# Kernel optimization log

Hardware: AMD Instinct MI355X
Metric: run time of the kernel (lower is better)

Reference implementation:

```python
import jax, jax.numpy as jnp
import numpy as np

GAMMA = 0.1
PENALTY = 0.0
BANDWIDTH = 1.0e6
B, N, M = 64, 512, 512


def setup_inputs() -> dict:
    key = jax.random.key(0)
    k1, k2, k3 = jax.random.split(key, 3)
    D = jax.random.uniform(k1, (B, N, M), dtype=jnp.float32)
    mask = jnp.ones((B, N, M), dtype=jnp.float32)
    # valid lengths in [N/2, N] so R[b, x_lens[b], y_lens[b]] is always reachable
    x_lens = jax.random.randint(k2, (B,), N // 2, N + 1)
    y_lens = jax.random.randint(k3, (B,), M // 2, M + 1)
    return {"D": D, "mask": mask, "x_lens": x_lens, "y_lens": y_lens}


def _softdtw(D, x_lens, y_lens):
    # Soft-DTW DP over anti-diagonals. D: [B, N, M] masked cost.
    # Returns per-batch loss R[b, x_lens[b], y_lens[b]].
    Bn, Nn, Mn = D.shape
    inv_gamma = 1.0 / GAMMA
    inf = jnp.float32(jnp.inf)
    ii = jnp.arange(Nn + 1)  # row index i = 0..N within a diagonal buffer
    im1 = jnp.clip(ii - 1, 0, Nn)
    # diagonal buffers: entry i of diag s holds R[i, s - i]
    d0 = jnp.full((Bn, Nn + 1), inf).at[:, 0].set(0.0)  # s=0: only R[0,0]=0
    d1 = jnp.full((Bn, Nn + 1), inf)                    # s=1: boundary, all inf
    xl = x_lens[:, None]
    yl = y_lens[:, None]

    def step(carry, s):
        dm2, dm1 = carry                      # diagonals s-2 and s-1
        jj = s - ii                           # column index j for each i
        r00 = dm2[:, im1]                     # R[i-1, j-1]
        r01 = dm1[:, im1]                     # R[i-1, j]
        r10 = dm1                             # R[i,   j-1]
        r0 = -r00 * inv_gamma
        r1 = -(r01 + PENALTY) * inv_gamma
        r2 = -(r10 + PENALTY) * inv_gamma
        rmax = jnp.maximum(jnp.maximum(r0, r1), r2)
        finite = jnp.isfinite(rmax)
        rs = jnp.where(finite, rmax, 0.0)     # safe max (avoid inf-inf -> nan)
        rsum = jnp.exp(r0 - rs) + jnp.exp(r1 - rs) + jnp.exp(r2 - rs)
        softmin = jnp.where(finite, -GAMMA * (jnp.log(rsum) + rs), inf)
        dcell = D[:, jnp.clip(ii - 1, 0, Nn - 1), jnp.clip(jj - 1, 0, Mn - 1)]
        new = dcell + softmin                 # R[i, j] = D[i-1, j-1] + softmin
        valid = (ii >= 1) & (ii <= Nn) & (jj >= 1) & (jj <= Mn)
        valid = valid & (jnp.abs(jj - ii) <= BANDWIDTH)
        upd = valid[None, :] & (ii[None, :] <= xl) & (jj[None, :] <= yl)
        dnew = jnp.where(upd, new, inf)
        return (dm1, dnew), dnew

    _, diags = jax.lax.scan(step, (d0, d1), jnp.arange(2, Nn + Mn + 1))
    # diags: [N+M-1, B, N+1]; diag index s-2 holds cells with i+j == s
    s_idx = jnp.clip(x_lens + y_lens - 2, 0, Nn + Mn - 2)
    loss = diags[s_idx, jnp.arange(Bn), x_lens]
    return loss


def reference(D, mask, x_lens, y_lens):
    return _softdtw(D * mask, x_lens, y_lens)
```

## Files before the change

### kernel.cpp

```cpp
#include <hip/hip_runtime.h>


constexpr int Bn = 64, Nn = 512, Mn = 512;
constexpr int TARGET_E = -30;

__device__ __forceinline__ float exp2_fast(float x) {
    float r; asm("v_exp_f32 %0, %1" : "=v"(r) : "v"(x)); return r;
}
__device__ __forceinline__ float log2_fast(float x) {
    float r; asm("v_log_f32 %0, %1" : "=v"(r) : "v"(x)); return r;
}
__device__ __forceinline__ float ldexp_fast(float x, int e) {
    float r; asm("v_ldexp_f32 %0, %1, %2" : "=v"(r) : "v"(x), "v"(e)); return r;
}
__device__ __forceinline__ int frexp_exp(float x) {
    int r; asm("v_frexp_exp_i32_f32 %0, %1" : "=v"(r) : "v"(x)); return r;
}

#define PLOAD(MM)                                                              \
    {   const int base_ = 4 * ((MM) - t);                                      \
        _Pragma("unroll")                                                      \
        for (int rr = 0; rr < 4; ++rr) {                                       \
            int r_ = min(max(base_ + rr, 0), Nn - 1);                          \
            int o_ = r_ * (Mn / 4) + chunk;                                    \
            pD[rr][0] = D4[o_];  pD[rr][1] = D4[o_ + 1];                       \
            pM[rr][0] = M4[o_];  pM[rr][1] = M4[o_ + 1];                       \
        } }

#define PBUILD(MM)                                                             \
    {   const int s_ = (MM) % 6;                                               \
        _Pragma("unroll")                                                      \
        for (int rr = 0; rr < 4; ++rr) {                                       \
            float4 p_ = pD[rr][0] * pM[rr][0] * negk;                          \
            float4 q_ = pD[rr][1] * pM[rr][1] * negk;                          \
            float4 wa_, wb_;                                                   \
            wa_.x = exp2_fast(p_.x);  wa_.y = exp2_fast(p_.y);                 \
            wa_.z = exp2_fast(p_.z);  wa_.w = exp2_fast(p_.w);                 \
            wb_.x = exp2_fast(q_.x);  wb_.y = exp2_fast(q_.y);                 \
            wb_.z = exp2_fast(q_.z);  wb_.w = exp2_fast(q_.w);                 \
            wlds[s_][2 * rr][t]     = wa_;                                     \
            wlds[s_][2 * rr + 1][t] = wb_;                                     \
        } }

#define CSTEP(MM, WCUR, WNXT)                                                  \
    {                                                                          \
        const int m_ = (MM);                                                   \
        {   const int sn_ = (m_ + 1) % 6;                                      \
            _Pragma("unroll")                                                  \
            for (int rr = 0; rr < 4; ++rr) {                                   \
                WNXT[rr][0] = wlds[sn_][2 * rr][t];                            \
                WNXT[rr][1] = wlds[sn_][2 * rr + 1][t];                        \
            } }                                                                \
        if (m_ <= 63) {                                   \
            if (m_ == t && t != 0) {                                           \
                _Pragma("unroll")                                              \
                for (int c = 0; c < 8; ++c) E[c] = 0.0f;                       \
                Ld = 0.0f;                                                     \
            }                                                                  \
        }                                                                      \
        float ce3_, co_[4];                                                    \
        _Pragma("unroll")                                                      \
        for (int rr = 0; rr < 4; ++rr) {                                       \
            const float Wr_[8] = {                                             \
                WCUR[rr][0].x, WCUR[rr][0].y, WCUR[rr][0].z, WCUR[rr][0].w,    \
                WCUR[rr][1].x, WCUR[rr][1].y, WCUR[rr][1].z, WCUR[rr][1].w };  \
            const float c0s_ = (rr == 0) ? Ld : L[rr - 1];                     \
            float c2_ = L[rr];                                                 \
            float A_[8], Bv_[8];                                               \
            A_[0] = E[0] + c0s_;                                               \
            _Pragma("unroll")                                                  \
            for (int c = 1; c < 8; ++c) A_[c] = E[c] + E[c - 1];               \
            _Pragma("unroll")                                                  \
            for (int c = 0; c < 8; ++c) Bv_[c] = Wr_[c] * A_[c];               \
            _Pragma("unroll")                                                  \
            for (int c = 0; c < 8; ++c) {                                      \
                float nv_ = fmaf(Wr_[c], c2_, Bv_[c]);                         \
                E[c] = nv_;  c2_ = nv_;                                        \
            }                                                                  \
            if (rr == 3) ce3_ = c2_;                                           \
            co_[rr] = __shfl_up(c2_, 1);                                       \
            if (m_ == m_out && rr == r_out) {         \
                float sel_ = E[0];                                             \
                if (c_out == 1) sel_ = E[1];  if (c_out == 2) sel_ = E[2];     \
                if (c_out == 3) sel_ = E[3];  if (c_out == 4) sel_ = E[4];     \
                if (c_out == 5) sel_ = E[5];  if (c_out == 6) sel_ = E[6];     \
                if (c_out == 7) sel_ = E[7];                                   \
                ov = sel_;  ovS = S;                                           \
            }                                                                  \
        }                                                                      \
        int So_ = __shfl_up(S, 1);                                             \
        int eo_ = frexp_exp(ce3_);                                             \
        int ei_ = frexp_exp(co_[3]) + (So_ - S);                               \
        bool own0_  = (ce3_ == 0.0f);                                          \
        bool incok_ = (t != 0) && (co_[3] != 0.0f);                            \
        int  eref_  = (incok_ && ((ei_ > eo_) || own0_)) ? ei_ : eo_;          \
        int  shift_ = (own0_ && !incok_) ? 0 : (TARGET_E - eref_);             \
        if (m_ < t) shift_ = S - So_;                \
        int Snew_ = S - shift_;                                                \
        _Pragma("unroll")                                                      \
        for (int c = 0; c < 8; ++c) E[c] = ldexp_fast(E[c], shift_);           \
        Ld = ldexp_fast(L[3], shift_);                                         \
        {   int d_ = So_ - Snew_;                                              \
            _Pragma("unroll")                                                  \
            for (int rr = 0; rr < 4; ++rr)                                     \
                L[rr] = (t == 0) ? 0.0f : ldexp_fast(co_[rr], d_);             \
        }                                                                      \
        S = Snew_;                                                             \
    }

__global__ __launch_bounds__(192) void softdtw_fwd(
    const float* __restrict__ D, const float* __restrict__ Msk,
    const int* __restrict__ xlens, const int* __restrict__ ylens,
    float* __restrict__ out)
{
    const int tid = threadIdx.x;
    const int w   = tid >> 6;
    const int t   = tid & 63;
    const int b   = blockIdx.x;
    const int xl = xlens[b];
    const int yl = ylens[b];
    const int t_out = (yl - 1) >> 3;
    const int c_out = (yl - 1) & 7;
    const int r_out = (xl - 1) & 3;
    const int m_out = ((xl - 1) >> 2) + t_out;
    const int nsuper = (m_out >> 1) + 1;

    const float negk = -14.4269504088896341f;
    const float klog = 0.06931471805599453f;

    __shared__ float4 wlds[6][8][64];

    const float4* __restrict__ D4 = (const float4*)(D   + (size_t)b * (Nn * Mn));
    const float4* __restrict__ M4 = (const float4*)(Msk + (size_t)b * (Nn * Mn));
    const int chunk = t * 2;

    float E[8];
#pragma unroll
    for (int c = 0; c < 8; ++c) E[c] = 0.0f;
    float L[4] = {0.0f, 0.0f, 0.0f, 0.0f};
    float Ld = (t == 0) ? 1.0f : 0.0f;
    int S = 0;
    float ov = 1.0f;  int ovS = 0;
    float4 Wc[4][2], Wn[4][2];

    float4 pD[4][2], pM[4][2];

    if (w == 1) {
        PLOAD(0); PBUILD(0);
        PLOAD(2); PBUILD(2);
        PLOAD(4);
    } else if (w == 2) {
        PLOAD(1); PBUILD(1);
        PLOAD(3); PBUILD(3);
        PLOAD(5);
    }
    __syncthreads();
    if (w == 0) {
#pragma unroll
        for (int rr = 0; rr < 4; ++rr) {
            Wc[rr][0] = wlds[0][2 * rr][t];
            Wc[rr][1] = wlds[0][2 * rr + 1][t];
        }
    }

    for (int u = 0; u < nsuper; ++u) {
        if (w == 0) {
            CSTEP(2 * u, Wc, Wn);
            if (2 * u + 1 <= m_out) CSTEP(2 * u + 1, Wn, Wc);
        } else if (w == 1) {
            PBUILD(2 * u + 4);
            PLOAD(2 * u + 6);
        } else {
            PBUILD(2 * u + 5);
            PLOAD(2 * u + 7);
        }
        __syncthreads();
    }

    if (w == 0 && t == t_out) {
        int   ev = frexp_exp(ov);
        float mv = ldexp_fast(ov, -ev);
        out[b] = -(log2_fast(mv) + (float)(ev + ovS)) * klog;
    }
}

extern "C" void kernel_launch(void* const* d_in, const int* in_sizes, int n_in,
                              void* d_out, int out_size, void* d_ws, size_t ws_size,
                              hipStream_t stream) {
    const float* D   = (const float*)d_in[0];
    const float* Msk = (const float*)d_in[1];
    const int*   xl  = (const int*)d_in[2];
    const int*   yl  = (const int*)d_in[3];
    float* out = (float*)d_out;
    softdtw_fwd<<<dim3(Bn), dim3(192), 0, stream>>>(D, Msk, xl, yl, out);
}
```

Measured before the change: 145.7 us.

## Replace per-step block barriers with LDS flag-based producer/consumer handoff

Result: slower. 172.0 us (+18.1%).

```diff
diff --git a/kernel.cpp b/kernel.cpp
--- a/kernel.cpp
+++ b/kernel.cpp
@@ -17,22 +17,29 @@
     int r; asm("v_frexp_exp_i32_f32 %0, %1" : "=v"(r) : "v"(x)); return r;
 }
 
-#define PLOAD(MM)                                                              \
+#define LGKM0() asm volatile("s_waitcnt lgkmcnt(0)" ::: "memory")
+#define SCHED_FENCE() __builtin_amdgcn_sched_barrier(0)
+
+#define PLOAD(MM, BD, BM)                                                      \
     {   const int base_ = 4 * ((MM) - t);                                      \
         _Pragma("unroll")                                                      \
         for (int rr = 0; rr < 4; ++rr) {                                       \
             int r_ = min(max(base_ + rr, 0), Nn - 1);                          \
             int o_ = r_ * (Mn / 4) + chunk;                                    \
-            pD[rr][0] = D4[o_];  pD[rr][1] = D4[o_ + 1];                       \
-            pM[rr][0] = M4[o_];  pM[rr][1] = M4[o_ + 1];                       \
+            BD[rr][0] = D4[o_];  BD[rr][1] = D4[o_ + 1];                       \
+            BM[rr][0] = M4[o_];  BM[rr][1] = M4[o_ + 1];                       \
         } }
 
-#define PBUILD(MM)                                                             \
-    {   const int s_ = (MM) % 6;                                               \
-        _Pragma("unroll")                                                      \
-        for (int rr = 0; rr < 4; ++rr) {                                       \
-            float4 p_ = pD[rr][0] * pM[rr][0] * negk;                          \
-            float4 q_ = pD[rr][1] * pM[rr][1] * negk;                          \
+#define PSTEP(MM, BD, BM)                                                      \
+    {                                                                          \
+        const int m_ = (MM);                                                   \
+        while (vcd[0] < m_ - 7) {}                                             \
+        SCHED_FENCE();                                                         \
+        const int s_ = m_ % 6;                                                 \
+        _Pragma("unroll")                                                      \
+        for (int rr = 0; rr < 4; ++rr) {                                       \
+            float4 p_ = BD[rr][0] * BM[rr][0] * negk;                          \
+            float4 q_ = BD[rr][1] * BM[rr][1] * negk;                          \
             float4 wa_, wb_;                                                   \
             wa_.x = exp2_fast(p_.x);  wa_.y = exp2_fast(p_.y);                 \
             wa_.z = exp2_fast(p_.z);  wa_.w = exp2_fast(p_.w);                 \
@@ -40,18 +47,24 @@
             wb_.z = exp2_fast(q_.z);  wb_.w = exp2_fast(q_.w);                 \
             wlds[s_][2 * rr][t]     = wa_;                                     \
             wlds[s_][2 * rr + 1][t] = wb_;                                     \
-        } }
+        }                                                                      \
+        LGKM0();                                                               \
+        if (t == 0) vfs[s_] = m_;                                              \
+        PLOAD(m_ + 4, BD, BM);                                                 \
+    }
 
 #define CSTEP(MM, WCUR, WNXT)                                                  \
     {                                                                          \
         const int m_ = (MM);                                                   \
-        {   const int sn_ = (m_ + 1) % 6;                                      \
-            _Pragma("unroll")                                                  \
-            for (int rr = 0; rr < 4; ++rr) {                                   \
-                WNXT[rr][0] = wlds[sn_][2 * rr][t];                            \
-                WNXT[rr][1] = wlds[sn_][2 * rr + 1][t];                        \
-            } }                                                                \
-        if (m_ <= 63) {                                   \
+        const int sn_ = (m_ + 1) % 6;                                          \
+        while (vfs[sn_] != m_ + 1) {}                                          \
+        SCHED_FENCE();                                                         \
+        _Pragma("unroll")                                                      \
+        for (int rr = 0; rr < 4; ++rr) {                                       \
+            WNXT[rr][0] = wlds[sn_][2 * rr][t];                                \
+            WNXT[rr][1] = wlds[sn_][2 * rr + 1][t];                            \
+        }                                                                      \
+        if (m_ <= 63) {                                                        \
             if (m_ == t && t != 0) {                                           \
                 _Pragma("unroll")                                              \
                 for (int c = 0; c < 8; ++c) E[c] = 0.0f;                       \
@@ -106,6 +119,8 @@
                 L[rr] = (t == 0) ? 0.0f : ldexp_fast(co_[rr], d_);             \
         }                                                                      \
         S = Snew_;                                                             \
+        LGKM0();                                                               \
+        if (t == 0) vcd[0] = m_;                                               \
     }
 
 __global__ __launch_bounds__(192) void softdtw_fwd(
@@ -123,64 +138,64 @@
     const int c_out = (yl - 1) & 7;
     const int r_out = (xl - 1) & 3;
     const int m_out = ((xl - 1) >> 2) + t_out;
-    const int nsuper = (m_out >> 1) + 1;
+    const int mlast = m_out + 1;
 
     const float negk = -14.4269504088896341f;
     const float klog = 0.06931471805599453f;
 
     __shared__ float4 wlds[6][8][64];
+    __shared__ int fslot[6];
+    __shared__ int cdone;
+    volatile int* vfs = fslot;
+    volatile int* vcd = &cdone;
+
+    if (tid < 6) fslot[tid] = -1;
+    if (tid == 6) cdone = -1;
+    __syncthreads();
 
     const float4* __restrict__ D4 = (const float4*)(D   + (size_t)b * (Nn * Mn));
     const float4* __restrict__ M4 = (const float4*)(Msk + (size_t)b * (Nn * Mn));
     const int chunk = t * 2;
 
-    float E[8];
+    if (w == 0) {
+        float E[8];
 #pragma unroll
-    for (int c = 0; c < 8; ++c) E[c] = 0.0f;
-    float L[4] = {0.0f, 0.0f, 0.0f, 0.0f};
-    float Ld = (t == 0) ? 1.0f : 0.0f;
-    int S = 0;
-    float ov = 1.0f;  int ovS = 0;
-    float4 Wc[4][2], Wn[4][2];
-
-    float4 pD[4][2], pM[4][2];
-
-    if (w == 1) {
-        PLOAD(0); PBUILD(0);
-        PLOAD(2); PBUILD(2);
-        PLOAD(4);
-    } else if (w == 2) {
-        PLOAD(1); PBUILD(1);
-        PLOAD(3); PBUILD(3);
-        PLOAD(5);
-    }
-    __syncthreads();
-    if (w == 0) {
+        for (int c = 0; c < 8; ++c) E[c] = 0.0f;
+        float L[4] = {0.0f, 0.0f, 0.0f, 0.0f};
+        float Ld = (t == 0) ? 1.0f : 0.0f;
+        int S = 0;
+        float ov = 1.0f;  int ovS = 0;
+        float4 Wc[4][2], Wn[4][2];
+
+        while (vfs[0] != 0) {}
+        SCHED_FENCE();
 #pragma unroll
         for (int rr = 0; rr < 4; ++rr) {
             Wc[rr][0] = wlds[0][2 * rr][t];
             Wc[rr][1] = wlds[0][2 * rr + 1][t];
         }
-    }
-
-    for (int u = 0; u < nsuper; ++u) {
-        if (w == 0) {
-            CSTEP(2 * u, Wc, Wn);
-            if (2 * u + 1 <= m_out) CSTEP(2 * u + 1, Wn, Wc);
-        } else if (w == 1) {
-            PBUILD(2 * u + 4);
-            PLOAD(2 * u + 6);
-        } else {
-            PBUILD(2 * u + 5);
-            PLOAD(2 * u + 7);
-        }
-        __syncthreads();
-    }
-
-    if (w == 0 && t == t_out) {
-        int   ev = frexp_exp(ov);
-        float mv = ldexp_fast(ov, -ev);
-        out[b] = -(log2_fast(mv) + (float)(ev + ovS)) * klog;
+
+        int m = 0;
+        for (; m + 1 <= m_out; m += 2) {
+            CSTEP(m,     Wc, Wn);
+            CSTEP(m + 1, Wn, Wc);
+        }
+        if (m <= m_out) CSTEP(m, Wc, Wn);
+
+        if (t == t_out) {
+            int   ev = frexp_exp(ov);
+            float mv = ldexp_fast(ov, -ev);
+            out[b] = -(log2_fast(mv) + (float)(ev + ovS)) * klog;
+        }
+    } else {
+        const int p = w - 1;
+        float4 pDa[4][2], pMa[4][2], pDb[4][2], pMb[4][2];
+        PLOAD(p,     pDa, pMa);
+        PLOAD(p + 2, pDb, pMb);
+        for (int mp = p; mp <= mlast; mp += 4) {
+            PSTEP(mp, pDa, pMa);
+            if (mp + 2 <= mlast) PSTEP(mp + 2, pDb, pMb);
+        }
     }
 }
 
```

## Widen per-lane tile to 8x8 and use four producer wavefronts

Applied to the files above, without the earlier changes.

Measured after the change: 223.9 us. 53.8% more time.

```diff
diff --git a/kernel.cpp b/kernel.cpp
--- a/kernel.cpp
+++ b/kernel.cpp
@@ -2,7 +2,7 @@
 
 
 constexpr int Bn = 64, Nn = 512, Mn = 512;
-constexpr int TARGET_E = -30;
+constexpr int TARGET_E = -8;
 
 __device__ __forceinline__ float exp2_fast(float x) {
     float r; asm("v_exp_f32 %0, %1" : "=v"(r) : "v"(x)); return r;
@@ -17,50 +17,51 @@
     int r; asm("v_frexp_exp_i32_f32 %0, %1" : "=v"(r) : "v"(x)); return r;
 }
 
-#define PLOAD(MM)                                                              \
-    {   const int base_ = 4 * ((MM) - t);                                      \
+#define PLOAD4(SLOT, RBASE, BD, BM)                                            \
+    {   const int base_ = 8 * ((SLOT) - t) + (RBASE);                          \
         _Pragma("unroll")                                                      \
         for (int rr = 0; rr < 4; ++rr) {                                       \
             int r_ = min(max(base_ + rr, 0), Nn - 1);                          \
             int o_ = r_ * (Mn / 4) + chunk;                                    \
-            pD[rr][0] = D4[o_];  pD[rr][1] = D4[o_ + 1];                       \
-            pM[rr][0] = M4[o_];  pM[rr][1] = M4[o_ + 1];                       \
+            BD[rr][0] = D4[o_];  BD[rr][1] = D4[o_ + 1];                       \
+            BM[rr][0] = M4[o_];  BM[rr][1] = M4[o_ + 1];                       \
         } }
 
-#define PBUILD(MM)                                                             \
-    {   const int s_ = (MM) % 6;                                               \
+#define PBUILD4(SLOT, RBASE, BD, BM)                                           \
+    {   const int s_ = (SLOT) & 3;                                             \
         _Pragma("unroll")                                                      \
         for (int rr = 0; rr < 4; ++rr) {                                       \
-            float4 p_ = pD[rr][0] * pM[rr][0] * negk;                          \
-            float4 q_ = pD[rr][1] * pM[rr][1] * negk;                          \
+            float4 p_ = BD[rr][0] * BM[rr][0] * negk;                          \
+            float4 q_ = BD[rr][1] * BM[rr][1] * negk;                          \
             float4 wa_, wb_;                                                   \
             wa_.x = exp2_fast(p_.x);  wa_.y = exp2_fast(p_.y);                 \
             wa_.z = exp2_fast(p_.z);  wa_.w = exp2_fast(p_.w);                 \
             wb_.x = exp2_fast(q_.x);  wb_.y = exp2_fast(q_.y);                 \
             wb_.z = exp2_fast(q_.z);  wb_.w = exp2_fast(q_.w);                 \
-            wlds[s_][2 * rr][t]     = wa_;                                     \
-            wlds[s_][2 * rr + 1][t] = wb_;                                     \
+            wlds[s_][2 * ((RBASE) + rr)][t]     = wa_;                         \
+            wlds[s_][2 * ((RBASE) + rr) + 1][t] = wb_;                         \
         } }
 
-#define CSTEP(MM, WCUR, WNXT)                                                  \
+#define CSTEP8(MM, WCUR, WNXT)                                                 \
     {                                                                          \
-        const int m_ = (MM);                                                   \
-        {   const int sn_ = (m_ + 1) % 6;                                      \
-            _Pragma("unroll")                                                  \
-            for (int rr = 0; rr < 4; ++rr) {                                   \
-                WNXT[rr][0] = wlds[sn_][2 * rr][t];                            \
-                WNXT[rr][1] = wlds[sn_][2 * rr + 1][t];                        \
-            } }                                                                \
-        if (m_ <= 63) {                                   \
+        const int m_  = (MM);                                                  \
+        const int sn_ = (m_ + 1) & 3;                                          \
+        _Pragma("unroll")                                                      \
+        for (int rr = 0; rr < 8; ++rr) {                                       \
+            WNXT[rr][0] = wlds[sn_][2 * rr][t];                                \
+            WNXT[rr][1] = wlds[sn_][2 * rr + 1][t];                            \
+        }                                                                      \
+        if (m_ <= 63) {                                                        \
             if (m_ == t && t != 0) {                                           \
                 _Pragma("unroll")                                              \
                 for (int c = 0; c < 8; ++c) E[c] = 0.0f;                       \
                 Ld = 0.0f;                                                     \
             }                                                                  \
         }                                                                      \
-        float ce3_, co_[4];                                                    \
-        _Pragma("unroll")                                                      \
-        for (int rr = 0; rr < 4; ++rr) {                                       \
+        float ce7_ = 0.0f;                                                     \
+        float co_[8];                                                          \
+        _Pragma("unroll")                                                      \
+        for (int rr = 0; rr < 8; ++rr) {                                       \
             const float Wr_[8] = {                                             \
                 WCUR[rr][0].x, WCUR[rr][0].y, WCUR[rr][0].z, WCUR[rr][0].w,    \
                 WCUR[rr][1].x, WCUR[rr][1].y, WCUR[rr][1].z, WCUR[rr][1].w };  \
@@ -77,38 +78,40 @@
                 float nv_ = fmaf(Wr_[c], c2_, Bv_[c]);                         \
                 E[c] = nv_;  c2_ = nv_;                                        \
             }                                                                  \
-            if (rr == 3) ce3_ = c2_;                                           \
+            if (rr == 7) ce7_ = c2_;                                           \
             co_[rr] = __shfl_up(c2_, 1);                                       \
-            if (m_ == m_out && rr == r_out) {         \
-                float sel_ = E[0];                                             \
-                if (c_out == 1) sel_ = E[1];  if (c_out == 2) sel_ = E[2];     \
-                if (c_out == 3) sel_ = E[3];  if (c_out == 4) sel_ = E[4];     \
-                if (c_out == 5) sel_ = E[5];  if (c_out == 6) sel_ = E[6];     \
-                if (c_out == 7) sel_ = E[7];                                   \
-                ov = sel_;  ovS = S;                                           \
+            if (m_ == m_out) {                       \
+                if (rr == r_out) {                                             \
+                    float sel_ = E[0];                                         \
+                    if (c_out == 1) sel_ = E[1];  if (c_out == 2) sel_ = E[2]; \
+                    if (c_out == 3) sel_ = E[3];  if (c_out == 4) sel_ = E[4]; \
+                    if (c_out == 5) sel_ = E[5];  if (c_out == 6) sel_ = E[6]; \
+                    if (c_out == 7) sel_ = E[7];                               \
+                    ov = sel_;  ovS = S;                                       \
+                }                                                              \
             }                                                                  \
         }                                                                      \
         int So_ = __shfl_up(S, 1);                                             \
-        int eo_ = frexp_exp(ce3_);                                             \
-        int ei_ = frexp_exp(co_[3]) + (So_ - S);                               \
-        bool own0_  = (ce3_ == 0.0f);                                          \
-        bool incok_ = (t != 0) && (co_[3] != 0.0f);                            \
+        int eo_ = frexp_exp(ce7_);                                             \
+        int ei_ = frexp_exp(co_[7]) + (So_ - S);                               \
+        bool own0_  = (ce7_ == 0.0f);                                          \
+        bool incok_ = (t != 0) && (co_[7] != 0.0f);                            \
         int  eref_  = (incok_ && ((ei_ > eo_) || own0_)) ? ei_ : eo_;          \
         int  shift_ = (own0_ && !incok_) ? 0 : (TARGET_E - eref_);             \
         if (m_ < t) shift_ = S - So_;                \
         int Snew_ = S - shift_;                                                \
         _Pragma("unroll")                                                      \
         for (int c = 0; c < 8; ++c) E[c] = ldexp_fast(E[c], shift_);           \
-        Ld = ldexp_fast(L[3], shift_);                                         \
+        Ld = ldexp_fast(L[7], shift_);                                         \
         {   int d_ = So_ - Snew_;                                              \
             _Pragma("unroll")                                                  \
-            for (int rr = 0; rr < 4; ++rr)                                     \
+            for (int rr = 0; rr < 8; ++rr)                                     \
                 L[rr] = (t == 0) ? 0.0f : ldexp_fast(co_[rr], d_);             \
         }                                                                      \
         S = Snew_;                                                             \
     }
 
-__global__ __launch_bounds__(192) void softdtw_fwd(
+__global__ __launch_bounds__(320, 1) void softdtw_fwd(
     const float* __restrict__ D, const float* __restrict__ Msk,
     const int* __restrict__ xlens, const int* __restrict__ ylens,
     float* __restrict__ out)
@@ -121,14 +124,14 @@
     const int yl = ylens[b];
     const int t_out = (yl - 1) >> 3;
     const int c_out = (yl - 1) & 7;
-    const int r_out = (xl - 1) & 3;
-    const int m_out = ((xl - 1) >> 2) + t_out;
+    const int r_out = (xl - 1) & 7;
+    const int m_out = ((xl - 1) >> 3) + t_out;
     const int nsuper = (m_out >> 1) + 1;
 
     const float negk = -14.4269504088896341f;
     const float klog = 0.06931471805599453f;
 
-    __shared__ float4 wlds[6][8][64];
+    __shared__ float4 wlds[4][16][64];
 
     const float4* __restrict__ D4 = (const float4*)(D   + (size_t)b * (Nn * Mn));
     const float4* __restrict__ M4 = (const float4*)(Msk + (size_t)b * (Nn * Mn));
@@ -137,27 +140,29 @@
     float E[8];
 #pragma unroll
     for (int c = 0; c < 8; ++c) E[c] = 0.0f;
-    float L[4] = {0.0f, 0.0f, 0.0f, 0.0f};
+    float L[8] = {0.0f, 0.0f, 0.0f, 0.0f, 0.0f, 0.0f, 0.0f, 0.0f};
     float Ld = (t == 0) ? 1.0f : 0.0f;
     int S = 0;
     float ov = 1.0f;  int ovS = 0;
-    float4 Wc[4][2], Wn[4][2];
-
-    float4 pD[4][2], pM[4][2];
-
-    if (w == 1) {
-        PLOAD(0); PBUILD(0);
-        PLOAD(2); PBUILD(2);
-        PLOAD(4);
-    } else if (w == 2) {
-        PLOAD(1); PBUILD(1);
-        PLOAD(3); PBUILD(3);
-        PLOAD(5);
+    float4 Wc[8][2], Wn[8][2];
+
+    const int q    = w - 1;
+    const int half = (q & 1) * 4;
+    const int ss   = q >> 1;
+    float4 bD0[4][2], bM0[4][2], bD1[4][2], bM1[4][2];
+
+    if (w != 0) {
+        if (q < 3) {
+            PLOAD4(q, 0, bD0, bM0);  PBUILD4(q, 0, bD0, bM0);
+            PLOAD4(q, 4, bD0, bM0);  PBUILD4(q, 4, bD0, bM0);
+        }
+        PLOAD4(3 + ss, half, bD1, bM1);
     }
     __syncthreads();
+
     if (w == 0) {
 #pragma unroll
-        for (int rr = 0; rr < 4; ++rr) {
+        for (int rr = 0; rr < 8; ++rr) {
             Wc[rr][0] = wlds[0][2 * rr][t];
             Wc[rr][1] = wlds[0][2 * rr + 1][t];
         }
@@ -165,14 +170,13 @@
 
     for (int u = 0; u < nsuper; ++u) {
         if (w == 0) {
-            CSTEP(2 * u, Wc, Wn);
-            if (2 * u + 1 <= m_out) CSTEP(2 * u + 1, Wn, Wc);
-        } else if (w == 1) {
-            PBUILD(2 * u + 4);
-            PLOAD(2 * u + 6);
+            CSTEP8(2 * u, Wc, Wn);
+            if (2 * u + 1 <= m_out) CSTEP8(2 * u + 1, Wn, Wc);
         } else {
-            PBUILD(2 * u + 5);
-            PLOAD(2 * u + 7);
+            if (u & 1) { PLOAD4(2 * u + 5 + ss, half, bD1, bM1);
+                         PBUILD4(2 * u + 3 + ss, half, bD0, bM0); }
+            else       { PLOAD4(2 * u + 5 + ss, half, bD0, bM0);
+                         PBUILD4(2 * u + 3 + ss, half, bD1, bM1); }
         }
         __syncthreads();
     }
@@ -192,5 +196,5 @@
     const int*   xl  = (const int*)d_in[2];
     const int*   yl  = (const int*)d_in[3];
     float* out = (float*)d_out;
-    softdtw_fwd<<<dim3(Bn), dim3(192), 0, stream>>>(D, Msk, xl, yl, out);
-}
+    softdtw_fwd<<<dim3(Bn), dim3(320), 0, stream>>>(D, Msk, xl, yl, out);
+}
```

## Double-buffer producer global loads and defer consumer LDS prefetch past compute

Applied to the files above, without the earlier changes.

Measured after the change: 155.5 us. +6.8%, slower.

```diff
diff --git a/kernel.cpp b/kernel.cpp
--- a/kernel.cpp
+++ b/kernel.cpp
@@ -17,22 +17,22 @@
     int r; asm("v_frexp_exp_i32_f32 %0, %1" : "=v"(r) : "v"(x)); return r;
 }
 
-#define PLOAD(MM)                                                              \
+#define PLOAD(MM, BD, BM)                                                      \
     {   const int base_ = 4 * ((MM) - t);                                      \
         _Pragma("unroll")                                                      \
         for (int rr = 0; rr < 4; ++rr) {                                       \
             int r_ = min(max(base_ + rr, 0), Nn - 1);                          \
             int o_ = r_ * (Mn / 4) + chunk;                                    \
-            pD[rr][0] = D4[o_];  pD[rr][1] = D4[o_ + 1];                       \
-            pM[rr][0] = M4[o_];  pM[rr][1] = M4[o_ + 1];                       \
+            BD[rr][0] = D4[o_];  BD[rr][1] = D4[o_ + 1];                       \
+            BM[rr][0] = M4[o_];  BM[rr][1] = M4[o_ + 1];                       \
         } }
 
-#define PBUILD(MM)                                                             \
+#define PBUILD(MM, BD, BM)                                                     \
     {   const int s_ = (MM) % 6;                                               \
         _Pragma("unroll")                                                      \
         for (int rr = 0; rr < 4; ++rr) {                                       \
-            float4 p_ = pD[rr][0] * pM[rr][0] * negk;                          \
-            float4 q_ = pD[rr][1] * pM[rr][1] * negk;                          \
+            float4 p_ = BD[rr][0] * BM[rr][0] * negk;                          \
+            float4 q_ = BD[rr][1] * BM[rr][1] * negk;                          \
             float4 wa_, wb_;                                                   \
             wa_.x = exp2_fast(p_.x);  wa_.y = exp2_fast(p_.y);                 \
             wa_.z = exp2_fast(p_.z);  wa_.w = exp2_fast(p_.w);                 \
@@ -45,13 +45,7 @@
 #define CSTEP(MM, WCUR, WNXT)                                                  \
     {                                                                          \
         const int m_ = (MM);                                                   \
-        {   const int sn_ = (m_ + 1) % 6;                                      \
-            _Pragma("unroll")                                                  \
-            for (int rr = 0; rr < 4; ++rr) {                                   \
-                WNXT[rr][0] = wlds[sn_][2 * rr][t];                            \
-                WNXT[rr][1] = wlds[sn_][2 * rr + 1][t];                        \
-            } }                                                                \
-        if (m_ <= 63) {                                   \
+        if (m_ <= 63) {                                                        \
             if (m_ == t && t != 0) {                                           \
                 _Pragma("unroll")                                              \
                 for (int c = 0; c < 8; ++c) E[c] = 0.0f;                       \
@@ -106,6 +100,12 @@
                 L[rr] = (t == 0) ? 0.0f : ldexp_fast(co_[rr], d_);             \
         }                                                                      \
         S = Snew_;                                                             \
+        {   const int sn_ = (m_ + 1) % 6;       \
+            _Pragma("unroll")                                                  \
+            for (int rr = 0; rr < 4; ++rr) {                                   \
+                WNXT[rr][0] = wlds[sn_][2 * rr][t];                            \
+                WNXT[rr][1] = wlds[sn_][2 * rr + 1][t];                        \
+            } }                                                                \
     }
 
 __global__ __launch_bounds__(192) void softdtw_fwd(
@@ -143,18 +143,16 @@
     float ov = 1.0f;  int ovS = 0;
     float4 Wc[4][2], Wn[4][2];
 
-    float4 pD[4][2], pM[4][2];
+    const int p = w - 1;
+    float4 bD0[4][2], bM0[4][2], bD1[4][2], bM1[4][2];
 
-    if (w == 1) {
-        PLOAD(0); PBUILD(0);
-        PLOAD(2); PBUILD(2);
-        PLOAD(4);
-    } else if (w == 2) {
-        PLOAD(1); PBUILD(1);
-        PLOAD(3); PBUILD(3);
-        PLOAD(5);
+    if (w != 0) {
+        PLOAD(p, bD0, bM0);      PBUILD(p, bD0, bM0);
+        PLOAD(p + 2, bD0, bM0);  PBUILD(p + 2, bD0, bM0);
+        PLOAD(4 + p, bD1, bM1);
     }
     __syncthreads();
+
     if (w == 0) {
 #pragma unroll
         for (int rr = 0; rr < 4; ++rr) {
@@ -167,12 +165,11 @@
         if (w == 0) {
             CSTEP(2 * u, Wc, Wn);
             if (2 * u + 1 <= m_out) CSTEP(2 * u + 1, Wn, Wc);
-        } else if (w == 1) {
-            PBUILD(2 * u + 4);
-            PLOAD(2 * u + 6);
         } else {
-            PBUILD(2 * u + 5);
-            PLOAD(2 * u + 7);
+            if (u & 1) { PLOAD(2 * u + 6 + p, bD1, bM1);
+                         PBUILD(2 * u + 4 + p, bD0, bM0); }
+            else       { PLOAD(2 * u + 6 + p, bD0, bM0);
+                         PBUILD(2 * u + 4 + p, bD1, bM1); }
         }
         __syncthreads();
     }
```
